# Kernel tuning notes

Measured on AMD Instinct MI355X. Metric: run time of the kernel, lower is better.

The kernel has to match this reference:

```python
import jax, jax.numpy as jnp
import numpy as np

HEADS = 16
DIM_HEAD = 64
SCALE = DIM_HEAD ** -0.5


def setup_inputs() -> dict:
    key = jax.random.key(0)
    k1, k2, k3 = jax.random.split(key, 3)
    B, N, D = 4, 4096, 1024
    inner = HEADS * DIM_HEAD  # 1024
    x = jax.random.normal(k1, (B, N, D), dtype=jnp.float32)
    w_qkv = jax.random.normal(k2, (D, 3 * inner), dtype=jnp.float32) * (D ** -0.5)
    w_out = jax.random.normal(k3, (inner, D), dtype=jnp.float32) * (inner ** -0.5)
    b_out = jnp.zeros((D,), dtype=jnp.float32)
    return {"x": x, "w_qkv": w_qkv, "w_out": w_out, "b_out": b_out}


def reference(x, w_qkv, w_out, b_out):
    B, N, D = x.shape
    inner = HEADS * DIM_HEAD
    qkv = x @ w_qkv  # [B, N, 3*inner]
    q, k, v = jnp.split(qkv, 3, axis=-1)

    def to_heads(t):  # [B, N, inner] -> [B, H, N, Dh]
        return t.reshape(B, N, HEADS, DIM_HEAD).transpose(0, 2, 1, 3)

    q, k, v = to_heads(q), to_heads(k), to_heads(v)
    q = jax.nn.softmax(q * SCALE, axis=-1)   # softmax over feature dim d
    k = jax.nn.softmax(k, axis=-2)           # softmax over sequence dim n
    # context[d, e] = sum_n q[n, d] * k[n, e]
    context = jnp.einsum('bhnd,bhne->bhde', q, k)
    # out[n, e] = sum_d context[d, e] * v[n, d]
    out = jnp.einsum('bhde,bhnd->bhne', context, v)
    out = out.transpose(0, 2, 1, 3).reshape(B, N, inner)  # [B, N, inner]
    return out @ w_out + b_out
```

## Files before the change

### kernel.cpp

```cpp
#include <hip/hip_runtime.h>
#include <hip/hip_bf16.h>

#define SEQ    4096
#define SCALE  0.125f

typedef __attribute__((ext_vector_type(8))) short s8v;
typedef __attribute__((ext_vector_type(4))) float f4v;

__device__ __forceinline__ unsigned short f2bf(float f){
  unsigned int u = __builtin_bit_cast(unsigned int, f);
  u += 0x7FFFu + ((u >> 16) & 1u);
  return (unsigned short)(u >> 16);
}

typedef const __attribute__((address_space(1))) unsigned int gl_uint;
typedef __attribute__((address_space(3))) unsigned int lds_uint;

__device__ __forceinline__ void gload_lds16(const unsigned short* g, unsigned short* l){
  __builtin_amdgcn_global_load_lds((gl_uint*)g, (lds_uint*)l, 16, 0, 0);
}

#define MM(a,b,c) __builtin_amdgcn_mfma_f32_16x16x32_bf16(a,b,c,0,0,0)
#define BAR() __builtin_amdgcn_s_barrier()
#define SB0() __builtin_amdgcn_sched_barrier(0)
#define VMW(n) asm volatile("s_waitcnt vmcnt(" #n ")" ::: "memory")

__device__ __forceinline__ void mfmaH0(const s8v (&A)[8], const s8v (&B)[4], f4v (&acc)[8][4]){
#pragma unroll
  for (int m = 0; m < 4; m++)
#pragma unroll
    for (int n = 0; n < 4; n++) acc[m][n] = MM(A[m], B[n], acc[m][n]);
}
__device__ __forceinline__ void mfmaH1(const s8v (&A)[8], const s8v (&B)[4], f4v (&acc)[8][4]){
#pragma unroll
  for (int m = 4; m < 8; m++)
#pragma unroll
    for (int n = 0; n < 4; n++) acc[m][n] = MM(A[m], B[n], acc[m][n]);
}

__device__ __forceinline__ void mainloop_256(
    const unsigned short* __restrict__ Ag,
    const unsigned short* __restrict__ Bg,
    int bm, int bn, f4v (&acc)[8][4])
{
  __shared__ __align__(16) unsigned short lds[65536];
  const int tid  = threadIdx.x;
  const int wave = tid >> 6, lane = tid & 63;
  const int quad = lane >> 4, l16 = lane & 15;
  const int wmi  = wave >> 2, wni = wave & 3;
  const char* ldsc = (const char*)lds;

  const int c16   = (quad ^ ((l16 >> 1) & 3)) * 16;
  const int abase = (wmi * 128 + l16) * 64 + c16;
  const int bbase = 16384 + (wni * 64 + l16) * 64 + c16;

  const int schunk = (((tid & 3) ^ ((tid >> 3) & 3)) * 8);
  const unsigned short* aS = Ag + (size_t)(bm + (tid >> 2)) * 1024 + schunk;
  const unsigned short* bS = Bg + (size_t)(bn + (tid >> 2)) * 1024 + schunk;
  unsigned short* ldsw = lds + wave * 512;

#define STG_A(t_) do{ unsigned short* d_ = ldsw + ((t_) & 3) * 16384; \
    const unsigned short* s_ = aS + (t_) * 32; \
    gload_lds16(s_, d_); gload_lds16(s_ + 128 * 1024, d_ + 4096); }while(0)
#define STG_B(t_) do{ unsigned short* d_ = ldsw + ((t_) & 3) * 16384 + 8192; \
    const unsigned short* s_ = bS + (t_) * 32; \
    gload_lds16(s_, d_); gload_lds16(s_ + 128 * 1024, d_ + 4096); }while(0)

#define LD_B4(NB, base_) do{ \
    NB[0] = *(const s8v*)((base_) + bbase);        NB[1] = *(const s8v*)((base_) + bbase + 1024); \
    NB[2] = *(const s8v*)((base_) + bbase + 2048); NB[3] = *(const s8v*)((base_) + bbase + 3072); }while(0)
#define LD_A4LO(NA, base_) do{ \
    NA[0] = *(const s8v*)((base_) + abase);        NA[1] = *(const s8v*)((base_) + abase + 1024); \
    NA[2] = *(const s8v*)((base_) + abase + 2048); NA[3] = *(const s8v*)((base_) + abase + 3072); }while(0)
#define LD_A4HI(NA, base_) do{ \
    NA[4] = *(const s8v*)((base_) + abase + 4096); NA[5] = *(const s8v*)((base_) + abase + 5120); \
    NA[6] = *(const s8v*)((base_) + abase + 6144); NA[7] = *(const s8v*)((base_) + abase + 7168); }while(0)

  s8v A0[8], B0[4], A1[8], B1[4];

  STG_A(0); STG_B(0); STG_A(1); STG_B(1); STG_A(2); STG_B(2);
  VMW(8); BAR();
  LD_B4(B0, ldsc); LD_A4LO(A0, ldsc); LD_A4HI(A0, ldsc);

#define BODY(T_, CA, CB, NA, NB, DOSTG, VMWx) do{ \
    VMWx; BAR(); SB0(); \
    if (DOSTG){ STG_A((T_) + 3); STG_B((T_) + 3); } \
    { const char* nb_ = ldsc + ((((T_) + 1) & 3) << 15); \
      LD_B4(NB, nb_); LD_A4LO(NA, nb_); \
      __builtin_amdgcn_s_setprio(1); mfmaH0(CA, CB, acc); __builtin_amdgcn_s_setprio(0); \
      LD_A4HI(NA, nb_); \
      __builtin_amdgcn_s_setprio(1); mfmaH1(CA, CB, acc); __builtin_amdgcn_s_setprio(0); } \
  }while(0)

  for (int t = 0; t < 28; t += 2){
    BODY(t,     A0, B0, A1, B1, 1, VMW(4));
    BODY(t + 1, A1, B1, A0, B0, 1, VMW(4));
  }
  BODY(28, A0, B0, A1, B1, 1, VMW(4));
  BODY(29, A1, B1, A0, B0, 0, VMW(4));
  BODY(30, A0, B0, A1, B1, 0, VMW(0));
  __builtin_amdgcn_s_setprio(1);
  mfmaH0(A1, B1, acc); mfmaH1(A1, B1, acc);
  __builtin_amdgcn_s_setprio(0);

#undef BODY
#undef LD_B4
#undef LD_A4LO
#undef LD_A4HI
#undef STG_A
#undef STG_B
}

__global__ __launch_bounds__(512, 2) void qkv_gemm(
    const unsigned short* __restrict__ A,
    const unsigned short* __restrict__ Bt,
    unsigned short* __restrict__ qt,
    unsigned short* __restrict__ kt,
    unsigned short* __restrict__ vb)
{
  const int id  = blockIdx.x;
  const int swz = (id & 7) * 96 + (id >> 3);
  const int bm  = (swz / 12) * 256, bn = (swz % 12) * 256;

  f4v acc[8][4];
#pragma unroll
  for (int i = 0; i < 8; i++)
#pragma unroll
    for (int j = 0; j < 4; j++) acc[i][j] = (f4v){0.f,0.f,0.f,0.f};

  mainloop_256(A, Bt, bm, bn, acc);

  const int tid = threadIdx.x;
  const int wave = tid >> 6, lane = tid & 63;
  const int quad = lane >> 4, l16 = lane & 15;
  const int wmi = wave >> 2, wni = wave & 3;
  const int colbase = bn + wni * 64;
  const int rowbase = bm + wmi * 128;
  const int sec = colbase >> 10;

  if (sec == 2){
#pragma unroll
    for (int nf = 0; nf < 4; nf++){
      int vc = colbase + nf * 16 + l16 - 2048;
#pragma unroll
      for (int mf = 0; mf < 8; mf++){
        int row = rowbase + mf * 16 + quad * 4;
#pragma unroll
        for (int r = 0; r < 4; r++)
          vb[(size_t)(row + r) * 1024 + vc] = f2bf(acc[mf][nf][r]);
      }
    }
    return;
  }

  if (sec == 0){
#pragma unroll
    for (int mf = 0; mf < 8; mf++){
#pragma unroll
      for (int r = 0; r < 4; r++){
        float m = fmaxf(fmaxf(acc[mf][0][r], acc[mf][1][r]),
                        fmaxf(acc[mf][2][r], acc[mf][3][r]));
        for (int off = 8; off; off >>= 1) m = fmaxf(m, __shfl_xor(m, off));
        m *= SCALE;
        float e0 = __expf(acc[mf][0][r] * SCALE - m);
        float e1 = __expf(acc[mf][1][r] * SCALE - m);
        float e2 = __expf(acc[mf][2][r] * SCALE - m);
        float e3 = __expf(acc[mf][3][r] * SCALE - m);
        float s = (e0 + e1) + (e2 + e3);
        for (int off = 8; off; off >>= 1) s += __shfl_xor(s, off);
        float inv = 1.f / s;
        acc[mf][0][r] = e0 * inv; acc[mf][1][r] = e1 * inv;
        acc[mf][2][r] = e2 * inv; acc[mf][3][r] = e3 * inv;
      }
    }
#pragma unroll
    for (int nf = 0; nf < 4; nf++){
      int col = colbase + nf * 16 + l16;
      int h = (col >> 6) & 15, de = col & 63;
#pragma unroll
      for (int mf = 0; mf < 8; mf++){
        int row = rowbase + mf * 16 + quad * 4;
        int bb = row >> 12, nl = row & 4095;
        ushort4 o;
        o.x = f2bf(acc[mf][nf][0]); o.y = f2bf(acc[mf][nf][1]);
        o.z = f2bf(acc[mf][nf][2]); o.w = f2bf(acc[mf][nf][3]);
        *(ushort4*)&qt[(((size_t)bb * 16 + h) * 64 + de) * SEQ + nl] = o;
      }
    }
  } else {
#pragma unroll
    for (int nf = 0; nf < 4; nf++){
      int col = colbase + nf * 16 + l16;
      int h = (col >> 6) & 15, de = col & 63;
#pragma unroll
      for (int mf = 0; mf < 8; mf++){
        int row = rowbase + mf * 16 + quad * 4;
        int bb = row >> 12, nl = row & 4095;
        ushort4 o;
        o.x = f2bf(__expf(acc[mf][nf][0])); o.y = f2bf(__expf(acc[mf][nf][1]));
        o.z = f2bf(__expf(acc[mf][nf][2])); o.w = f2bf(__expf(acc[mf][nf][3]));
        *(ushort4*)&kt[(((size_t)bb * 16 + h) * 64 + de) * SEQ + nl] = o;
      }
    }
  }
}

__global__ __launch_bounds__(512, 2) void gemm_final(
    const unsigned short* __restrict__ A,
    const unsigned short* __restrict__ C2t,
    float* __restrict__ Cf,
    const float* __restrict__ bias)
{
  const int id  = blockIdx.x;
  const int swz = (id & 7) * 32 + (id >> 3);
  const int bm  = (swz >> 2) * 256, bn = (swz & 3) * 256;
  const unsigned short* Bt = C2t + (size_t)(bm >> 12) * 1024 * 1024;

  f4v acc[8][4];
#pragma unroll
  for (int i = 0; i < 8; i++)
#pragma unroll
    for (int j = 0; j < 4; j++) acc[i][j] = (f4v){0.f,0.f,0.f,0.f};

  mainloop_256(A, Bt, bm, bn, acc);

  const int tid = threadIdx.x;
  const int wave = tid >> 6, lane = tid & 63;
  const int quad = lane >> 4, l16 = lane & 15;
  const int wmi = wave >> 2, wni = wave & 3;

#pragma unroll
  for (int nf = 0; nf < 4; nf++){
    int col = bn + wni * 64 + nf * 16 + l16;
    float bv = bias[col];
#pragma unroll
    for (int mf = 0; mf < 8; mf++){
      int row = bm + wmi * 128 + mf * 16 + quad * 4;
#pragma unroll
      for (int r = 0; r < 4; r++)
        Cf[(size_t)(row + r) * 1024 + col] = acc[mf][nf][r] + bv;
    }
  }
}

__global__ void cvt_f32_bf16(const float4* __restrict__ in, ushort4* __restrict__ outp){
  int i = blockIdx.x * 256 + threadIdx.x;
  float4 v = in[i];
  ushort4 o;
  o.x = f2bf(v.x); o.y = f2bf(v.y); o.z = f2bf(v.z); o.w = f2bf(v.w);
  outp[i] = o;
}

__global__ __launch_bounds__(256) void transpose_cvt(const float* __restrict__ in,
                                                     unsigned short* __restrict__ outp,
                                                     int R, int C){
  __shared__ float tile[64][65];
  int r0 = blockIdx.y * 64, c0 = blockIdx.x * 64;
  int t = threadIdx.x;
  for (int i = t; i < 4096; i += 256){ int r = i >> 6, c = i & 63;
    tile[r][c] = in[(size_t)(r0 + r) * C + c0 + c]; }
  __syncthreads();
  for (int i = t; i < 4096; i += 256){ int c = i >> 6, r = i & 63;
    outp[(size_t)(c0 + c) * R + r0 + r] = f2bf(tile[r][c]); }
}

__global__ __launch_bounds__(256) void ctx_partial(const unsigned short* __restrict__ qt,
                                                   const unsigned short* __restrict__ kt,
                                                   float* __restrict__ ctxp){
  __shared__ float red[4096];
  int bh = blockIdx.x >> 2, ch = blockIdx.x & 3;
  int t = threadIdx.x, wave = t >> 6, lane = t & 63, quad = lane >> 4, l16 = lane & 15;
  const unsigned short* qb = qt + (size_t)bh * 64 * SEQ;
  const unsigned short* kb = kt + (size_t)bh * 64 * SEQ;
  f4v acc[4][4];
#pragma unroll
  for (int i = 0; i < 4; i++)
#pragma unroll
    for (int j = 0; j < 4; j++) acc[i][j] = (f4v){0.f,0.f,0.f,0.f};
  int ns = ch * 1024 + wave * 256;
  for (int n0 = ns; n0 < ns + 256; n0 += 32){
    s8v af[4], bf[4];
#pragma unroll
    for (int mt = 0; mt < 4; mt++) af[mt] = *(const s8v*)&qb[(size_t)(mt*16 + l16) * SEQ + n0 + quad*8];
#pragma unroll
    for (int nt = 0; nt < 4; nt++) bf[nt] = *(const s8v*)&kb[(size_t)(nt*16 + l16) * SEQ + n0 + quad*8];
#pragma unroll
    for (int mt = 0; mt < 4; mt++)
#pragma unroll
      for (int nt = 0; nt < 4; nt++)
        acc[mt][nt] = __builtin_amdgcn_mfma_f32_16x16x32_bf16(af[mt], bf[nt], acc[mt][nt], 0, 0, 0);
  }
  for (int i = t; i < 4096; i += 256) red[i] = 0.f;
  __syncthreads();
  for (int w = 0; w < 4; w++){
    if (wave == w){
#pragma unroll
      for (int mt = 0; mt < 4; mt++)
#pragma unroll
        for (int nt = 0; nt < 4; nt++)
#pragma unroll
          for (int r = 0; r < 4; r++)
            red[(mt*16 + quad*4 + r) * 64 + nt*16 + l16] += acc[mt][nt][r];
    }
    __syncthreads();
  }
  float* cp = ctxp + (size_t)blockIdx.x * 4096;
  for (int i = t; i < 4096; i += 256) cp[i] = red[i];
}

__global__ __launch_bounds__(256) void ctx2_kernel(const float* __restrict__ ctxp,
                                                   const float* __restrict__ w_out,
                                                   unsigned short* __restrict__ ctx2t){
  __shared__ float ctxs[4096];
  __shared__ float inv_s[64];
  int bh = blockIdx.x >> 4, fc = blockIdx.x & 15;
  int b = bh >> 4, h = bh & 15;
  int t = threadIdx.x;
  int fl = t & 63, dg = t >> 6;
  int f = fc * 64 + fl;
  for (int i = t; i < 4096; i += 256){
    const float* p = ctxp + (size_t)bh * 4 * 4096 + i;
    ctxs[i] = (p[0] + p[4096]) + (p[8192] + p[12288]);
  }
  __syncthreads();
  if (t < 64){
    float s = 0.f;
#pragma unroll
    for (int d = 0; d < 64; d++) s += ctxs[d * 64 + t];
    inv_s[t] = 1.f / s;
  }
  __syncthreads();
  float acc[16];
#pragma unroll
  for (int i = 0; i < 16; i++) acc[i] = 0.f;
  for (int e = 0; e < 64; e++){
    float w = w_out[(size_t)(h * 64 + e) * 1024 + f] * inv_s[e];
#pragma unroll
    for (int dd = 0; dd < 16; dd++)
      acc[dd] += ctxs[(dg * 16 + dd) * 64 + e] * w;
  }
  unsigned short* op = ctx2t + ((size_t)b * 1024 + f) * 1024 + h * 64 + dg * 16;
#pragma unroll
  for (int g = 0; g < 4; g++){
    ushort4 o;
    o.x = f2bf(acc[g*4+0]); o.y = f2bf(acc[g*4+1]);
    o.z = f2bf(acc[g*4+2]); o.w = f2bf(acc[g*4+3]);
    *(ushort4*)&op[g*4] = o;
  }
}

extern "C" void kernel_launch(void* const* d_in, const int* in_sizes, int n_in,
                              void* d_out, int out_size, void* d_ws, size_t ws_size,
                              hipStream_t stream) {
  const float* x     = (const float*)d_in[0];
  const float* w_qkv = (const float*)d_in[1];
  const float* w_out = (const float*)d_in[2];
  const float* b_out = (const float*)d_in[3];
  float* out = (float*)d_out;

  const int M = 4 * SEQ;

  unsigned short* xb = (unsigned short*)d_out;

  char* wp = (char*)d_ws;
  size_t off = 0;
  auto nxt = [&](size_t bytes) -> char* {
    char* p = wp + off;
    off += (bytes + 255) & ~(size_t)255;
    return p;
  };
  unsigned short* wqkvT = (unsigned short*)nxt((size_t)3072 * 1024 * 2);
  unsigned short* qt    = (unsigned short*)nxt((size_t)64 * 64 * SEQ * 2);
  unsigned short* kt    = (unsigned short*)nxt((size_t)64 * 64 * SEQ * 2);
  unsigned short* vb    = (unsigned short*)nxt((size_t)M * 1024 * 2);
  float*          ctxp  = (float*)wqkvT;
  unsigned short* ctx2t = qt;

  cvt_f32_bf16<<<(M * 1024) / 4 / 256, 256, 0, stream>>>((const float4*)x, (ushort4*)xb);
  transpose_cvt<<<dim3(3072 / 64, 1024 / 64), 256, 0, stream>>>(w_qkv, wqkvT, 1024, 3072);

  qkv_gemm<<<768, 512, 0, stream>>>(xb, wqkvT, qt, kt, vb);

  ctx_partial<<<64 * 4, 256, 0, stream>>>(qt, kt, ctxp);

  ctx2_kernel<<<64 * 16, 256, 0, stream>>>(ctxp, w_out, ctx2t);

  gemm_final<<<256, 512, 0, stream>>>(vb, ctx2t, out, b_out);
}
```

Measured before the change: 349.1 us.

## Pre-pack B operands in MFMA fragment layout and load them directly from global

The weight matrix and the ctx2 matrix are now written in a fragment-packed layout that matches the MFMA B-operand register layout. The GEMM mainloop then loads B straight from global memory into registers instead of staging it through LDS, which halves LDS usage and removes the B LDS reads. The pipeline is restructured to match, with new wait counts and an extra loop body replacing the tail. The risk is that the B global-load latency is no longer hidden by the multi-stage LDS buffering, since each B fragment is loaded only one step ahead and re-read by every block sharing that bn.

```diff
diff --git a/kernel.cpp b/kernel.cpp
--- a/kernel.cpp
+++ b/kernel.cpp
@@ -5,6 +5,7 @@
 #define SCALE  0.125f
 
 typedef __attribute__((ext_vector_type(8))) short s8v;
+typedef __attribute__((ext_vector_type(8))) unsigned short u8v;
 typedef __attribute__((ext_vector_type(4))) float f4v;
 
 __device__ __forceinline__ unsigned short f2bf(float f){
@@ -40,10 +41,10 @@
 
 __device__ __forceinline__ void mainloop_256(
     const unsigned short* __restrict__ Ag,
-    const unsigned short* __restrict__ Bg,
+    const unsigned short* __restrict__ Bpk,
     int bm, int bn, f4v (&acc)[8][4])
 {
-  __shared__ __align__(16) unsigned short lds[65536];
+  __shared__ __align__(16) unsigned short lds[32768];
   const int tid  = threadIdx.x;
   const int wave = tid >> 6, lane = tid & 63;
   const int quad = lane >> 4, l16 = lane & 15;
@@ -52,68 +53,66 @@
 
   const int c16   = (quad ^ ((l16 >> 1) & 3)) * 16;
   const int abase = (wmi * 128 + l16) * 64 + c16;
-  const int bbase = 16384 + (wni * 64 + l16) * 64 + c16;
 
   const int schunk = (((tid & 3) ^ ((tid >> 3) & 3)) * 8);
   const unsigned short* aS = Ag + (size_t)(bm + (tid >> 2)) * 1024 + schunk;
-  const unsigned short* bS = Bg + (size_t)(bn + (tid >> 2)) * 1024 + schunk;
   unsigned short* ldsw = lds + wave * 512;
 
-#define STG_A(t_) do{ unsigned short* d_ = ldsw + ((t_) & 3) * 16384; \
+  const unsigned short* bP = Bpk + ((size_t)((bn >> 4) + wni * 4) * 2048 + lane) * 8;
+
+#define STG_A(t_) do{ unsigned short* d_ = ldsw + ((t_) & 3) * 8192; \
     const unsigned short* s_ = aS + (t_) * 32; \
     gload_lds16(s_, d_); gload_lds16(s_ + 128 * 1024, d_ + 4096); }while(0)
-#define STG_B(t_) do{ unsigned short* d_ = ldsw + ((t_) & 3) * 16384 + 8192; \
-    const unsigned short* s_ = bS + (t_) * 32; \
-    gload_lds16(s_, d_); gload_lds16(s_ + 128 * 1024, d_ + 4096); }while(0)
-
-#define LD_B4(NB, base_) do{ \
-    NB[0] = *(const s8v*)((base_) + bbase);        NB[1] = *(const s8v*)((base_) + bbase + 1024); \
-    NB[2] = *(const s8v*)((base_) + bbase + 2048); NB[3] = *(const s8v*)((base_) + bbase + 3072); }while(0)
-#define LD_A4LO(NA, base_) do{ \
-    NA[0] = *(const s8v*)((base_) + abase);        NA[1] = *(const s8v*)((base_) + abase + 1024); \
-    NA[2] = *(const s8v*)((base_) + abase + 2048); NA[3] = *(const s8v*)((base_) + abase + 3072); }while(0)
-#define LD_A4HI(NA, base_) do{ \
-    NA[4] = *(const s8v*)((base_) + abase + 4096); NA[5] = *(const s8v*)((base_) + abase + 5120); \
-    NA[6] = *(const s8v*)((base_) + abase + 6144); NA[7] = *(const s8v*)((base_) + abase + 7168); }while(0)
+
+#define LDB(t_, BN) do{ \
+    BN[0] = *(const s8v*)(bP +         (t_) * 512); \
+    BN[1] = *(const s8v*)(bP + 16384 + (t_) * 512); \
+    BN[2] = *(const s8v*)(bP + 32768 + (t_) * 512); \
+    BN[3] = *(const s8v*)(bP + 49152 + (t_) * 512); }while(0)
+
+#define LD_A4LO(NA, base_) do{ const char* p_ = (base_); \
+    NA[0] = *(const s8v*)(p_ + abase);        NA[1] = *(const s8v*)(p_ + abase + 1024); \
+    NA[2] = *(const s8v*)(p_ + abase + 2048); NA[3] = *(const s8v*)(p_ + abase + 3072); }while(0)
+#define LD_A4HI(NA, base_) do{ const char* p_ = (base_); \
+    NA[4] = *(const s8v*)(p_ + abase + 4096); NA[5] = *(const s8v*)(p_ + abase + 5120); \
+    NA[6] = *(const s8v*)(p_ + abase + 6144); NA[7] = *(const s8v*)(p_ + abase + 7168); }while(0)
 
   s8v A0[8], B0[4], A1[8], B1[4];
 
-  STG_A(0); STG_B(0); STG_A(1); STG_B(1); STG_A(2); STG_B(2);
+  STG_A(0); STG_A(1); STG_A(2);
+  LDB(0, B0);
   VMW(8); BAR();
-  LD_B4(B0, ldsc); LD_A4LO(A0, ldsc); LD_A4HI(A0, ldsc);
-
-#define BODY(T_, CA, CB, NA, NB, DOSTG, VMWx) do{ \
-    VMWx; BAR(); SB0(); \
-    if (DOSTG){ STG_A((T_) + 3); STG_B((T_) + 3); } \
-    { const char* nb_ = ldsc + ((((T_) + 1) & 3) << 15); \
-      LD_B4(NB, nb_); LD_A4LO(NA, nb_); \
-      __builtin_amdgcn_s_setprio(1); mfmaH0(CA, CB, acc); __builtin_amdgcn_s_setprio(0); \
-      LD_A4HI(NA, nb_); \
-      __builtin_amdgcn_s_setprio(1); mfmaH1(CA, CB, acc); __builtin_amdgcn_s_setprio(0); } \
+  LD_A4LO(A0, ldsc); LD_A4HI(A0, ldsc);
+
+#define BODY(T_, CA, CB, NA, NB, DOSTG, DOLD) do{ \
+    SB0(); VMW(6); BAR(); SB0(); \
+    if (DOSTG) STG_A((T_) + 3); \
+    if (DOLD)  LDB((T_) + 1, NB); \
+    if (DOLD)  LD_A4LO(NA, ldsc + ((((T_) + 1) & 3) << 14)); \
+    __builtin_amdgcn_s_setprio(1); mfmaH0(CA, CB, acc); __builtin_amdgcn_s_setprio(0); \
+    if (DOLD)  LD_A4HI(NA, ldsc + ((((T_) + 1) & 3) << 14)); \
+    __builtin_amdgcn_s_setprio(1); mfmaH1(CA, CB, acc); __builtin_amdgcn_s_setprio(0); \
   }while(0)
 
   for (int t = 0; t < 28; t += 2){
-    BODY(t,     A0, B0, A1, B1, 1, VMW(4));
-    BODY(t + 1, A1, B1, A0, B0, 1, VMW(4));
-  }
-  BODY(28, A0, B0, A1, B1, 1, VMW(4));
-  BODY(29, A1, B1, A0, B0, 0, VMW(4));
-  BODY(30, A0, B0, A1, B1, 0, VMW(0));
-  __builtin_amdgcn_s_setprio(1);
-  mfmaH0(A1, B1, acc); mfmaH1(A1, B1, acc);
-  __builtin_amdgcn_s_setprio(0);
+    BODY(t,     A0, B0, A1, B1, 1, 1);
+    BODY(t + 1, A1, B1, A0, B0, 1, 1);
+  }
+  BODY(28, A0, B0, A1, B1, 1, 1);
+  BODY(29, A1, B1, A0, B0, 0, 1);
+  BODY(30, A0, B0, A1, B1, 0, 1);
+  BODY(31, A1, B1, A0, B0, 0, 0);
 
 #undef BODY
-#undef LD_B4
 #undef LD_A4LO
 #undef LD_A4HI
+#undef LDB
 #undef STG_A
-#undef STG_B
 }
 
 __global__ __launch_bounds__(512, 2) void qkv_gemm(
     const unsigned short* __restrict__ A,
-    const unsigned short* __restrict__ Bt,
+    const unsigned short* __restrict__ Bpk,
     unsigned short* __restrict__ qt,
     unsigned short* __restrict__ kt,
     unsigned short* __restrict__ vb)
@@ -128,7 +127,7 @@
 #pragma unroll
     for (int j = 0; j < 4; j++) acc[i][j] = (f4v){0.f,0.f,0.f,0.f};
 
-  mainloop_256(A, Bt, bm, bn, acc);
+  mainloop_256(A, Bpk, bm, bn, acc);
 
   const int tid = threadIdx.x;
   const int wave = tid >> 6, lane = tid & 63;
@@ -207,14 +206,14 @@
 
 __global__ __launch_bounds__(512, 2) void gemm_final(
     const unsigned short* __restrict__ A,
-    const unsigned short* __restrict__ C2t,
+    const unsigned short* __restrict__ C2pk,
     float* __restrict__ Cf,
     const float* __restrict__ bias)
 {
   const int id  = blockIdx.x;
   const int swz = (id & 7) * 32 + (id >> 3);
   const int bm  = (swz >> 2) * 256, bn = (swz & 3) * 256;
-  const unsigned short* Bt = C2t + (size_t)(bm >> 12) * 1024 * 1024;
+  const unsigned short* Bpk = C2pk + (size_t)(bm >> 12) * 1024 * 1024;
 
   f4v acc[8][4];
 #pragma unroll
@@ -222,7 +221,7 @@
 #pragma unroll
     for (int j = 0; j < 4; j++) acc[i][j] = (f4v){0.f,0.f,0.f,0.f};
 
-  mainloop_256(A, Bt, bm, bn, acc);
+  mainloop_256(A, Bpk, bm, bn, acc);
 
   const int tid = threadIdx.x;
   const int wave = tid >> 6, lane = tid & 63;
@@ -251,17 +250,24 @@
   outp[i] = o;
 }
 
-__global__ __launch_bounds__(256) void transpose_cvt(const float* __restrict__ in,
-                                                     unsigned short* __restrict__ outp,
-                                                     int R, int C){
+__global__ __launch_bounds__(256) void pack_w(const float* __restrict__ in,
+                                              unsigned short* __restrict__ outp){
   __shared__ float tile[64][65];
-  int r0 = blockIdx.y * 64, c0 = blockIdx.x * 64;
+  int c0 = blockIdx.x * 64, k0 = blockIdx.y * 64;
   int t = threadIdx.x;
-  for (int i = t; i < 4096; i += 256){ int r = i >> 6, c = i & 63;
-    tile[r][c] = in[(size_t)(r0 + r) * C + c0 + c]; }
+  for (int i = t; i < 4096; i += 256){ int k = i >> 6, c = i & 63;
+    tile[k][c] = in[(size_t)(k0 + k) * 3072 + c0 + c]; }
   __syncthreads();
-  for (int i = t; i < 4096; i += 256){ int c = i >> 6, r = i & 63;
-    outp[(size_t)(c0 + c) * R + r0 + r] = f2bf(tile[r][c]); }
+  for (int j = t; j < 512; j += 256){
+    int c_l = j & 63, k8 = j >> 6;
+    int c = c0 + c_l, k = k0 + k8 * 8;
+    u8v o;
+#pragma unroll
+    for (int e = 0; e < 8; e++) o[e] = f2bf(tile[k8 * 8 + e][c_l]);
+    size_t idx = ((size_t)(c >> 4) * 2048 + (size_t)(k >> 5) * 64 +
+                  ((k >> 3) & 3) * 16 + (c & 15)) * 8;
+    *(u8v*)&outp[idx] = o;
+  }
 }
 
 __global__ __launch_bounds__(256) void ctx_partial(const unsigned short* __restrict__ qt,
@@ -339,13 +345,16 @@
     for (int dd = 0; dd < 16; dd++)
       acc[dd] += ctxs[(dg * 16 + dd) * 64 + e] * w;
   }
-  unsigned short* op = ctx2t + ((size_t)b * 1024 + f) * 1024 + h * 64 + dg * 16;
+  unsigned short* base = ctx2t + (size_t)b * 1024 * 1024;
 #pragma unroll
   for (int g = 0; g < 4; g++){
+    int k = h * 64 + dg * 16 + g * 4;
+    int kt = k >> 5, quad = (k >> 3) & 3, e0 = k & 7;
+    size_t idx = ((size_t)(f >> 4) * 2048 + (size_t)kt * 64 + quad * 16 + (f & 15)) * 8 + e0;
     ushort4 o;
     o.x = f2bf(acc[g*4+0]); o.y = f2bf(acc[g*4+1]);
     o.z = f2bf(acc[g*4+2]); o.w = f2bf(acc[g*4+3]);
-    *(ushort4*)&op[g*4] = o;
+    *(ushort4*)&base[idx] = o;
   }
 }
 
@@ -369,17 +378,17 @@
     off += (bytes + 255) & ~(size_t)255;
     return p;
   };
-  unsigned short* wqkvT = (unsigned short*)nxt((size_t)3072 * 1024 * 2);
+  unsigned short* wqkvP = (unsigned short*)nxt((size_t)3072 * 1024 * 2);
   unsigned short* qt    = (unsigned short*)nxt((size_t)64 * 64 * SEQ * 2);
   unsigned short* kt    = (unsigned short*)nxt((size_t)64 * 64 * SEQ * 2);
   unsigned short* vb    = (unsigned short*)nxt((size_t)M * 1024 * 2);
-  float*          ctxp  = (float*)wqkvT;
+  float*          ctxp  = (float*)wqkvP;
   unsigned short* ctx2t = qt;
 
   cvt_f32_bf16<<<(M * 1024) / 4 / 256, 256, 0, stream>>>((const float4*)x, (ushort4*)xb);
-  transpose_cvt<<<dim3(3072 / 64, 1024 / 64), 256, 0, stream>>>(w_qkv, wqkvT, 1024, 3072);
-
-  qkv_gemm<<<768, 512, 0, stream>>>(xb, wqkvT, qt, kt, vb);
+  pack_w<<<dim3(3072 / 64, 1024 / 64), 256, 0, stream>>>(w_qkv, wqkvP);
+
+  qkv_gemm<<<768, 512, 0, stream>>>(xb, wqkvP, qt, kt, vb);
 
   ctx_partial<<<64 * 4, 256, 0, stream>>>(qt, kt, ctxp);
 
```

Result: faster. 339.6 us (-2.7%).

## Pre-pack final GEMM B operand in MFMA fragment order and load directly to registers

Applied to the files above, without the earlier changes.

The context kernel now writes the per-batch combined weight in a packed layout that matches the MFMA B-fragment order. The final GEMM gets a new mainloop that loads B straight from global memory into registers, skipping LDS staging, and keeps only A in a smaller LDS ring buffer. This removes LDS traffic and barriers for B and halves LDS use, which could allow more occupancy. The cost is uncoalesced-looking per-lane global loads for B, whose latency is exposed without LDS buffering.

```diff
diff --git a/kernel.cpp b/kernel.cpp
--- a/kernel.cpp
+++ b/kernel.cpp
@@ -5,6 +5,7 @@
 #define SCALE  0.125f
 
 typedef __attribute__((ext_vector_type(8))) short s8v;
+typedef __attribute__((ext_vector_type(8))) unsigned short u8v;
 typedef __attribute__((ext_vector_type(4))) float f4v;
 
 __device__ __forceinline__ unsigned short f2bf(float f){
@@ -38,7 +39,7 @@
     for (int n = 0; n < 4; n++) acc[m][n] = MM(A[m], B[n], acc[m][n]);
 }
 
-__device__ __forceinline__ void mainloop_256(
+__device__ __forceinline__ void mainloop_ab(
     const unsigned short* __restrict__ Ag,
     const unsigned short* __restrict__ Bg,
     int bm, int bn, f4v (&acc)[8][4])
@@ -111,6 +112,77 @@
 #undef STG_B
 }
 
+__device__ __forceinline__ void mainloop_apk(
+    const unsigned short* __restrict__ Ag,
+    const unsigned short* __restrict__ Bpk,
+    int bm, int bn, f4v (&acc)[8][4])
+{
+  __shared__ __align__(16) unsigned short lds[32768];
+  const int tid  = threadIdx.x;
+  const int wave = tid >> 6, lane = tid & 63;
+  const int quad = lane >> 4, l16 = lane & 15;
+  const int wmi  = wave >> 2, wni = wave & 3;
+  const char* ldsc = (const char*)lds;
+
+  const int c16   = (quad ^ ((l16 >> 1) & 3)) * 16;
+  const int abase = (wmi * 128 + l16) * 64 + c16;
+
+  const int schunk = (((tid & 3) ^ ((tid >> 3) & 3)) * 8);
+  const unsigned short* aS = Ag + (size_t)(bm + (tid >> 2)) * 1024 + schunk;
+  unsigned short* ldsw = lds + wave * 512;
+
+  const unsigned short* bP = Bpk + ((size_t)((bn >> 4) + wni * 4) * 2048 + lane) * 8;
+
+#define STG_A2(t_) do{ unsigned short* d_ = ldsw + ((t_) & 3) * 8192; \
+    const unsigned short* s_ = aS + (t_) * 32; \
+    gload_lds16(s_, d_); gload_lds16(s_ + 128 * 1024, d_ + 4096); }while(0)
+
+#define LDB2(t_, BN) do{ \
+    BN[0] = *(const s8v*)(bP +         (t_) * 512); \
+    BN[1] = *(const s8v*)(bP + 16384 + (t_) * 512); \
+    BN[2] = *(const s8v*)(bP + 32768 + (t_) * 512); \
+    BN[3] = *(const s8v*)(bP + 49152 + (t_) * 512); }while(0)
+
+#define LD2_A4LO(NA, base_) do{ const char* p_ = (base_); \
+    NA[0] = *(const s8v*)(p_ + abase);        NA[1] = *(const s8v*)(p_ + abase + 1024); \
+    NA[2] = *(const s8v*)(p_ + abase + 2048); NA[3] = *(const s8v*)(p_ + abase + 3072); }while(0)
+#define LD2_A4HI(NA, base_) do{ const char* p_ = (base_); \
+    NA[4] = *(const s8v*)(p_ + abase + 4096); NA[5] = *(const s8v*)(p_ + abase + 5120); \
+    NA[6] = *(const s8v*)(p_ + abase + 6144); NA[7] = *(const s8v*)(p_ + abase + 7168); }while(0)
+
+  s8v A0[8], B0[4], A1[8], B1[4];
+
+  STG_A2(0); STG_A2(1); STG_A2(2);
+  LDB2(0, B0);
+  VMW(8); BAR();
+  LD2_A4LO(A0, ldsc); LD2_A4HI(A0, ldsc);
+
+#define BODY2(T_, CA, CB, NA, NB, DOSTG, DOLD) do{ \
+    SB0(); VMW(6); BAR(); SB0(); \
+    if (DOSTG) STG_A2((T_) + 3); \
+    if (DOLD)  LDB2((T_) + 1, NB); \
+    if (DOLD)  LD2_A4LO(NA, ldsc + ((((T_) + 1) & 3) << 14)); \
+    __builtin_amdgcn_s_setprio(1); mfmaH0(CA, CB, acc); __builtin_amdgcn_s_setprio(0); \
+    if (DOLD)  LD2_A4HI(NA, ldsc + ((((T_) + 1) & 3) << 14)); \
+    __builtin_amdgcn_s_setprio(1); mfmaH1(CA, CB, acc); __builtin_amdgcn_s_setprio(0); \
+  }while(0)
+
+  for (int t = 0; t < 28; t += 2){
+    BODY2(t,     A0, B0, A1, B1, 1, 1);
+    BODY2(t + 1, A1, B1, A0, B0, 1, 1);
+  }
+  BODY2(28, A0, B0, A1, B1, 1, 1);
+  BODY2(29, A1, B1, A0, B0, 0, 1);
+  BODY2(30, A0, B0, A1, B1, 0, 1);
+  BODY2(31, A1, B1, A0, B0, 0, 0);
+
+#undef BODY2
+#undef LD2_A4LO
+#undef LD2_A4HI
+#undef LDB2
+#undef STG_A2
+}
+
 __global__ __launch_bounds__(512, 2) void qkv_gemm(
     const unsigned short* __restrict__ A,
     const unsigned short* __restrict__ Bt,
@@ -128,7 +200,7 @@
 #pragma unroll
     for (int j = 0; j < 4; j++) acc[i][j] = (f4v){0.f,0.f,0.f,0.f};
 
-  mainloop_256(A, Bt, bm, bn, acc);
+  mainloop_ab(A, Bt, bm, bn, acc);
 
   const int tid = threadIdx.x;
   const int wave = tid >> 6, lane = tid & 63;
@@ -207,14 +279,14 @@
 
 __global__ __launch_bounds__(512, 2) void gemm_final(
     const unsigned short* __restrict__ A,
-    const unsigned short* __restrict__ C2t,
+    const unsigned short* __restrict__ C2pk,
     float* __restrict__ Cf,
     const float* __restrict__ bias)
 {
   const int id  = blockIdx.x;
   const int swz = (id & 7) * 32 + (id >> 3);
   const int bm  = (swz >> 2) * 256, bn = (swz & 3) * 256;
-  const unsigned short* Bt = C2t + (size_t)(bm >> 12) * 1024 * 1024;
+  const unsigned short* Bpk = C2pk + (size_t)(bm >> 12) * 1024 * 1024;
 
   f4v acc[8][4];
 #pragma unroll
@@ -222,7 +294,7 @@
 #pragma unroll
     for (int j = 0; j < 4; j++) acc[i][j] = (f4v){0.f,0.f,0.f,0.f};
 
-  mainloop_256(A, Bt, bm, bn, acc);
+  mainloop_apk(A, Bpk, bm, bn, acc);
 
   const int tid = threadIdx.x;
   const int wave = tid >> 6, lane = tid & 63;
@@ -339,13 +411,16 @@
     for (int dd = 0; dd < 16; dd++)
       acc[dd] += ctxs[(dg * 16 + dd) * 64 + e] * w;
   }
-  unsigned short* op = ctx2t + ((size_t)b * 1024 + f) * 1024 + h * 64 + dg * 16;
+  unsigned short* base = ctx2t + (size_t)b * 1024 * 1024;
 #pragma unroll
   for (int g = 0; g < 4; g++){
+    int k = h * 64 + dg * 16 + g * 4;
+    int kt = k >> 5, quad = (k >> 3) & 3, e0 = k & 7;
+    size_t idx = ((size_t)(f >> 4) * 2048 + (size_t)kt * 64 + quad * 16 + (f & 15)) * 8 + e0;
     ushort4 o;
     o.x = f2bf(acc[g*4+0]); o.y = f2bf(acc[g*4+1]);
     o.z = f2bf(acc[g*4+2]); o.w = f2bf(acc[g*4+3]);
-    *(ushort4*)&op[g*4] = o;
+    *(ushort4*)&base[idx] = o;
   }
 }
 
```

New measurement: 342.3 us. About the same (-1.9%).
